# Kernel tuning notes

Measured on AMD Instinct MI355X. Metric: run time of the kernel, lower is better.

Reference implementation:

```python
import jax, jax.numpy as jnp
import numpy as np

C = 64          # out_C
IN_C = 2 * C    # in_C
B, H, W = 4, 64, 64


def conv_bn_relu(x, w, s, b):
    # 3x3 conv (stride 1, pad 1, no bias) + folded BatchNorm affine + ReLU
    y = jax.lax.conv_general_dilated(
        x, w, window_strides=(1, 1), padding=((1, 1), (1, 1)),
        dimension_numbers=("NCHW", "OIHW", "NCHW"))
    return jax.nn.relu(y * s[None, :, None, None] + b[None, :, None, None])


def attend(K, V, Q):
    # K, V, Q: [B, C, H, W]; mask = softmax(K^T Q) over last dim; out = V @ mask^T
    b, c, h, w = V.shape
    n = h * w
    Kf = K.reshape(b, c, n)
    Vf = V.reshape(b, c, n)
    Qf = Q.reshape(b, c, n)
    mask = jax.nn.softmax(jnp.einsum("bcn,bcm->bnm", Kf, Qf), axis=-1)  # [B,N,N]
    ref = jnp.einsum("bcn,bmn->bcm", Vf, mask)                          # V @ mask^T
    return ref.reshape(b, c, h, w)


def _conv_params(key, cin, cout):
    k1, k2, k3 = jax.random.split(key, 3)
    w = jax.random.normal(k1, (cout, cin, 3, 3), jnp.float32) * (1.0 / np.sqrt(cin * 9))
    s = jax.random.uniform(k2, (cout,), jnp.float32, 0.5, 1.5)   # folded BN scale
    bb = jax.random.normal(k3, (cout,), jnp.float32) * 0.1       # folded BN shift
    return w, s, bb


def setup_inputs() -> dict:
    key = jax.random.key(0)
    ks = jax.random.split(key, 9)
    x = jax.random.normal(ks[0], (B, C, H, W), jnp.float32)
    y = jax.random.normal(ks[1], (B, C, H, W), jnp.float32)
    q_w, q_s, q_b = _conv_params(ks[2], IN_C, C)
    rk_w, rk_s, rk_b = _conv_params(ks[3], C, C)
    rv_w, rv_s, rv_b = _conv_params(ks[4], C, C)
    ik_w, ik_s, ik_b = _conv_params(ks[5], C, C)
    iv_w, iv_s, iv_b = _conv_params(ks[6], C, C)
    sr_w, sr_s, sr_b = _conv_params(ks[7], IN_C, C)
    g1 = jax.random.normal(jax.random.fold_in(ks[8], 1), (1,), jnp.float32) * 0.1
    g2 = jax.random.normal(jax.random.fold_in(ks[8], 2), (1,), jnp.float32) * 0.1
    return dict(x=x, y=y,
                q_w=q_w, q_s=q_s, q_b=q_b,
                rk_w=rk_w, rk_s=rk_s, rk_b=rk_b,
                rv_w=rv_w, rv_s=rv_s, rv_b=rv_b,
                ik_w=ik_w, ik_s=ik_s, ik_b=ik_b,
                iv_w=iv_w, iv_s=iv_s, iv_b=iv_b,
                sr_w=sr_w, sr_s=sr_s, sr_b=sr_b,
                gamma1=g1, gamma2=g2)


def reference(x, y, q_w, q_s, q_b, rk_w, rk_s, rk_b, rv_w, rv_s, rv_b,
              ik_w, ik_s, ik_b, iv_w, iv_s, iv_b, sr_w, sr_s, sr_b,
              gamma1, gamma2):
    Q = conv_bn_relu(jnp.concatenate([x, y], axis=1), q_w, q_s, q_b)
    rgb_k = conv_bn_relu(x, rk_w, rk_s, rk_b)
    rgb_v = conv_bn_relu(x, rv_w, rv_s, rv_b)
    rgb_refine = gamma1[0] * attend(rgb_k, rgb_v, Q) + y
    inf_k = conv_bn_relu(y, ik_w, ik_s, ik_b)
    inf_v = conv_bn_relu(y, iv_w, iv_s, iv_b)
    inf_refine = gamma2[0] * attend(inf_k, inf_v, Q) + x
    out = conv_bn_relu(jnp.concatenate([rgb_refine, inf_refine], axis=1), sr_w, sr_s, sr_b)
    return out
```

## Files before the change

kernel.cpp:

```cpp
#include <hip/hip_runtime.h>
#include <hip/hip_bf16.h>

#define NPOS 4096
#define CD   64
#define NB   4
#define PADW 66
#define PADN (66*66)
#define NSEG 4
#define NT   (NPOS / NSEG / 64)
#define LOG2E 1.4426950408889634f

extern "C" __device__ float __ocml_exp2_f32(float);

typedef __bf16 bf16x8_t __attribute__((ext_vector_type(8)));
typedef float  f32x4_t  __attribute__((ext_vector_type(4)));

static __device__ __forceinline__ unsigned short f2bf(float f) {
    return __builtin_bit_cast(unsigned short, __float2bfloat16(f));
}

static __device__ __forceinline__ void gload_lds16(const void* g, void* l) {
    __builtin_amdgcn_global_load_lds(
        (const __attribute__((address_space(1))) void*)g,
        (__attribute__((address_space(3))) void*)l, 16, 0, 0);
}

static __device__ __forceinline__ unsigned cvtpk_bf16(float lo, float hi) {
    unsigned r;
    asm("v_cvt_pk_bf16_f32 %0, %1, %2" : "=v"(r) : "v"(lo), "v"(hi));
    return r;
}

__global__ __launch_bounds__(256) void prep_kernel(
    const float* __restrict__ x, const float* __restrict__ y,
    const float* __restrict__ qw, const float* __restrict__ rkw,
    const float* __restrict__ rvw, const float* __restrict__ ikw,
    const float* __restrict__ ivw, const float* __restrict__ srw,
    const float* __restrict__ qs, const float* __restrict__ rks,
    const float* __restrict__ rvs, const float* __restrict__ iks,
    const float* __restrict__ ivs, const float* __restrict__ srs,
    unsigned short* __restrict__ pads, unsigned short* __restrict__ Wf)
{
    const int bx = blockIdx.x;
    if (bx < 16) {
        unsigned short* p = pads + (size_t)bx * PADN * CD;
        const uint4 z = make_uint4(0, 0, 0, 0);
        for (int idx = threadIdx.x; idx < 260 * 8; idx += 256) {
            const int pi = idx >> 3, chn = idx & 7;
            int pos;
            if (pi < 66)       pos = pi;
            else if (pi < 132) pos = 65 * PADW + (pi - 66);
            else { const int rem = pi - 132;
                   pos = (1 + (rem >> 1)) * PADW + ((rem & 1) ? 65 : 0); }
            *(uint4*)(p + (size_t)pos * CD + chn * 8) = z;
        }
        return;
    }
    if (bx < 160) {
        const int f = bx - 16;
        const float* w; const float* s; int cin, local;
        if (f < 36)       { w = qw;  s = qs;  cin = 128; local = f; }
        else if (f < 54)  { w = rkw; s = rks; cin = 64;  local = f - 36; }
        else if (f < 72)  { w = rvw; s = rvs; cin = 64;  local = f - 54; }
        else if (f < 90)  { w = ikw; s = iks; cin = 64;  local = f - 72; }
        else if (f < 108) { w = ivw; s = ivs; cin = 64;  local = f - 90; }
        else              { w = srw; s = srs; cin = 128; local = f - 108; }
        const int src = (cin == 128) ? local / 18 : 0;
        const int rem = (cin == 128) ? local % 18 : local;
        const int tap = rem >> 1, kt = rem & 1;
        const int t = threadIdx.x, cot = t >> 6, l = t & 63;
        const int co = cot * 16 + (l & 15);
        const float kmul = ((f >= 36 && f < 54) || (f >= 72 && f < 90)) ? LOG2E : 1.0f;
        const float sc = s[co] * kmul;
        unsigned short us[8];
#pragma unroll
        for (int e = 0; e < 8; ++e) {
            const int ci = src * 64 + kt * 32 + ((l >> 4) * 8) + e;
            us[e] = f2bf(w[((size_t)co * cin + ci) * 9 + tap] * sc);
        }
        *(uint4*)(Wf + ((size_t)(f * 4 + cot) * 64 + l) * 8) = *(uint4*)us;
        return;
    }
    {
        const int idx = bx - 160;
        const int h = idx & 63, b = (idx >> 6) & 3, src = idx >> 8;
        const float* in = src ? y : x;
        unsigned short* out = pads + (size_t)src * NB * PADN * CD;
        __shared__ float t[64][65];
        const int tt = threadIdx.x;
        {
            const int ci = tt >> 2, w0 = (tt & 3) * 16;
            const float* p = in + ((size_t)b * 64 + ci) * NPOS + h * 64 + w0;
#pragma unroll
            for (int j = 0; j < 16; j += 4) {
                float4 v = *(const float4*)(p + j);
                t[ci][w0 + j] = v.x; t[ci][w0 + j + 1] = v.y;
                t[ci][w0 + j + 2] = v.z; t[ci][w0 + j + 3] = v.w;
            }
        }
        __syncthreads();
        const int w = tt >> 2, c0 = (tt & 3) * 16;
        unsigned short us[16];
#pragma unroll
        for (int j = 0; j < 16; ++j) us[j] = f2bf(t[c0 + j][w]);
        unsigned short* q = out + ((size_t)b * PADN + (h + 1) * PADW + (w + 1)) * CD + c0;
        *(uint4*)q = *(uint4*)us;
        *(uint4*)(q + 8) = *(uint4*)(us + 8);
    }
}

__global__ __launch_bounds__(256) void conv_mfma_kernel(
    const unsigned short* __restrict__ xpad, const unsigned short* __restrict__ ypad,
    const unsigned short* __restrict__ rpadR, const unsigned short* __restrict__ rpadI,
    const unsigned short* __restrict__ Wf,
    const float* __restrict__ qb, const float* __restrict__ rkb,
    const float* __restrict__ rvb, const float* __restrict__ ikb,
    const float* __restrict__ ivb, const float* __restrict__ srb,
    unsigned short* __restrict__ Qt, unsigned short* __restrict__ KtR,
    unsigned short* __restrict__ VR, unsigned short* __restrict__ KtI,
    unsigned short* __restrict__ VI, float* __restrict__ outf,
    int convid_base)
{
    const int conv = convid_base + (blockIdx.z >> 1);
    const int ch   = blockIdx.z & 1;
    const int rp = blockIdx.x, b = blockIdx.y;
    const unsigned short *in0, *in1; const float* bias;
    int nsrc, wfbase, layout; void* outp;
    switch (conv) {
        case 0:  in0 = xpad;  in1 = ypad;  nsrc = 2; wfbase = 0;   bias = qb;  outp = Qt;  layout = 0; break;
        case 1:  in0 = xpad;  in1 = 0;     nsrc = 1; wfbase = 36;  bias = rkb; outp = KtR; layout = 0; break;
        case 2:  in0 = xpad;  in1 = 0;     nsrc = 1; wfbase = 54;  bias = rvb; outp = VR;  layout = 1; break;
        case 3:  in0 = ypad;  in1 = 0;     nsrc = 1; wfbase = 72;  bias = ikb; outp = KtI; layout = 0; break;
        case 4:  in0 = ypad;  in1 = 0;     nsrc = 1; wfbase = 90;  bias = ivb; outp = VI;  layout = 1; break;
        default: in0 = rpadR; in1 = rpadI; nsrc = 2; wfbase = 108; bias = srb; outp = outf; layout = 2; break;
    }
    const float bmul = (conv == 1 || conv == 3) ? LOG2E : 1.0f;
    const int lane = threadIdx.x & 63, wv = threadIdx.x >> 6;
    const int l15 = lane & 15, g = lane >> 4;
    const int hrow = rp * 2 + (wv >> 1);
    const int posg = (wv & 1) * 32;

    __shared__ unsigned short Wl[12 * 512];

    f32x4_t acc[2][2];
#pragma unroll
    for (int i = 0; i < 2; ++i)
#pragma unroll
        for (int j = 0; j < 2; ++j) acc[i][j] = (f32x4_t){0.f, 0.f, 0.f, 0.f};

    const int nchunk = nsrc * 3;
    for (int c = 0; c < nchunk; ++c) {
        const int src = (c >= 3) ? 1 : 0;
        const int ky  = c - src * 3;
        if (c) __syncthreads();
#pragma unroll
        for (int j = 0; j < 3; ++j) {
            const int slot = wv * 3 + j;
            const int fj = slot >> 1, cotl = slot & 1;
            const int fg = wfbase + c * 6 + fj;
            gload_lds16(Wf + ((size_t)(fg * 4 + ch * 2 + cotl) * 64 + lane) * 8,
                        Wl + slot * 512);
        }
        __syncthreads();
        const unsigned short* base = (src ? in1 : in0) + (size_t)b * PADN * CD;
#pragma unroll
        for (int pf = 0; pf < 2; ++pf) {
#pragma unroll
            for (int kx = 0; kx < 3; ++kx) {
                const int pos = (hrow + ky) * PADW + posg + pf * 16 + kx + l15;
                const unsigned short* ap = base + (size_t)pos * CD + g * 8;
#pragma unroll
                for (int kt = 0; kt < 2; ++kt) {
                    bf16x8_t a = *(const bf16x8_t*)(ap + kt * 32);
                    const int fj = kx * 2 + kt;
#pragma unroll
                    for (int cc = 0; cc < 2; ++cc) {
                        bf16x8_t bfr = *(const bf16x8_t*)(Wl + (size_t)(fj * 2 + cc) * 512 + lane * 8);
                        acc[pf][cc] = __builtin_amdgcn_mfma_f32_16x16x32_bf16(a, bfr, acc[pf][cc], 0, 0, 0);
                    }
                }
            }
        }
    }

#pragma unroll
    for (int pf = 0; pf < 2; ++pf) {
        const int nb4 = hrow * 64 + posg + pf * 16 + g * 4;
        if (layout == 0) {
            unsigned short* o = (unsigned short*)outp + (size_t)b * NPOS * CD;
#pragma unroll
            for (int cc = 0; cc < 2; ++cc) {
                const int co = (ch * 2 + cc) * 16 + l15;
                const float bv = bias[co] * bmul;
#pragma unroll
                for (int r = 0; r < 4; ++r)
                    o[(size_t)(nb4 + r) * CD + co] = f2bf(fmaxf(acc[pf][cc][r] + bv, 0.f));
            }
        } else if (layout == 1) {
            unsigned short* o = (unsigned short*)outp + (size_t)b * CD * NPOS;
#pragma unroll
            for (int cc = 0; cc < 2; ++cc) {
                const int cch = (ch * 2 + cc) * 16 + l15;
                const float bv = bias[cch];
                unsigned short us[4];
#pragma unroll
                for (int r = 0; r < 4; ++r) us[r] = f2bf(fmaxf(acc[pf][cc][r] + bv, 0.f));
                *(uint2*)(o + (size_t)cch * NPOS + nb4) = *(uint2*)us;
            }
        } else {
            float* o = (float*)outp + (size_t)b * CD * NPOS;
#pragma unroll
            for (int cc = 0; cc < 2; ++cc) {
                const int cch = (ch * 2 + cc) * 16 + l15;
                const float bv = bias[cch];
                f32x4_t v;
#pragma unroll
                for (int r = 0; r < 4; ++r) v[r] = fmaxf(acc[pf][cc][r] + bv, 0.f);
                *(f32x4_t*)(o + (size_t)cch * NPOS + nb4) = v;
            }
        }
    }
}

__global__ __launch_bounds__(256) void attn_kernel(
    const unsigned short* __restrict__ Qt,
    const unsigned short* __restrict__ KtR, const unsigned short* __restrict__ KtI,
    const unsigned short* __restrict__ VR,  const unsigned short* __restrict__ VI,
    float* __restrict__ Opart, float* __restrict__ ml)
{
    const int fid = blockIdx.x;
    const int att = fid & 1;
    const int b   = (fid >> 1) & 3;
    const int seg = (fid >> 3) & 3;
    const int mblk = fid >> 5;
    const int lane = threadIdx.x & 63, wv = threadIdx.x >> 6;
    const int l15 = lane & 15, g = lane >> 4;
    const int m0 = mblk * 64 + wv * 16;

    const unsigned short* Qb = Qt + (size_t)b * NPOS * CD;
    const unsigned short* Kb = (att ? KtI : KtR) + (size_t)b * NPOS * CD;
    const unsigned short* Vb = (att ? VI : VR) + (size_t)b * CD * NPOS;

    __shared__ unsigned short Qs[2][64 * 64];
    __shared__ unsigned short Vs[2][64 * 64];
    __shared__ unsigned short plds[4][16 * 68];
    unsigned short* pl = plds[wv];

    const bf16x8_t bK0 = *(const bf16x8_t*)&Kb[(size_t)(m0 + l15) * CD + g * 8];
    const bf16x8_t bK1 = *(const bf16x8_t*)&Kb[(size_t)(m0 + l15) * CD + 32 + g * 8];

    f32x4_t O[4];
#pragma unroll
    for (int i = 0; i < 4; ++i) O[i] = (f32x4_t){0.f, 0.f, 0.f, 0.f};
    float mrun = -3.0e38f, lsum = 0.f;

    const int csw = (lane & 7) ^ ((lane >> 3) & 7);
    const int sx = l15 & 7;
    const int nbase = seg * (NPOS / NSEG);

    const int rq = wv * 16 + (lane >> 3);
    const unsigned short* qsrc0 = Qb + (size_t)(nbase + rq) * CD + csw * 8;
    const unsigned short* qsrc1 = qsrc0 + (size_t)8 * CD;
    const unsigned short* vsrc0 = Vb + (size_t)rq * NPOS + nbase + csw * 8;
    const unsigned short* vsrc1 = vsrc0 + (size_t)8 * NPOS;
    unsigned short* qdst = &Qs[0][(wv * 16) * 64];
    unsigned short* vdst = &Vs[0][(wv * 16) * 64];

#define STAGE(buf, itv) do {                                                  \
        const size_t qo = (size_t)(itv) * (64 * CD);                          \
        const size_t vo = (size_t)(itv) * 64;                                 \
        gload_lds16(qsrc0 + qo, qdst + (buf) * 4096);                         \
        gload_lds16(qsrc1 + qo, qdst + (buf) * 4096 + 512);                   \
        gload_lds16(vsrc0 + vo, vdst + (buf) * 4096);                         \
        gload_lds16(vsrc1 + vo, vdst + (buf) * 4096 + 512);                   \
    } while (0)

    STAGE(0, 0);

    for (int it = 0; it < NT; ++it) {
        const int cur = it & 1;
        __syncthreads();
        if (it + 1 < NT) STAGE(cur ^ 1, it + 1);

        f32x4_t St[4];
        __builtin_amdgcn_s_setprio(1);
#pragma unroll
        for (int nt = 0; nt < 4; ++nt) {
            const unsigned short* qr = &Qs[cur][(nt * 16 + l15) * 64];
            bf16x8_t a0 = *(const bf16x8_t*)(qr + (g ^ sx) * 8);
            bf16x8_t a1 = *(const bf16x8_t*)(qr + ((4 + g) ^ sx) * 8);
            f32x4_t c = (f32x4_t){0.f, 0.f, 0.f, 0.f};
            c = __builtin_amdgcn_mfma_f32_16x16x32_bf16(a0, bK0, c, 0, 0, 0);
            c = __builtin_amdgcn_mfma_f32_16x16x32_bf16(a1, bK1, c, 0, 0, 0);
            St[nt] = c;
        }
        __builtin_amdgcn_s_setprio(0);

        float tmax = St[0][0];
#pragma unroll
        for (int nt = 0; nt < 4; ++nt) {
            tmax = fmaxf(fmaxf(tmax, St[nt][0]), St[nt][1]);
            tmax = fmaxf(fmaxf(tmax, St[nt][2]), St[nt][3]);
        }
        if (!__all(tmax <= mrun + 12.0f)) {
            float tr = fmaxf(tmax, __shfl_xor(tmax, 16));
            tr = fmaxf(tr, __shfl_xor(tr, 32));
            const float mnew = fmaxf(mrun, tr);
            const float corr = __builtin_amdgcn_exp2f(mrun - mnew);
            lsum *= corr;
#pragma unroll
            for (int i = 0; i < 4; ++i) {
                O[i][0] *= corr; O[i][1] *= corr; O[i][2] *= corr; O[i][3] *= corr;
            }
            mrun = mnew;
        }
        unsigned int pw[8];
#pragma unroll
        for (int nt = 0; nt < 4; ++nt) {
            float p0 = __builtin_amdgcn_exp2f(St[nt][0] - mrun);
            float p1 = __builtin_amdgcn_exp2f(St[nt][1] - mrun);
            float p2 = __builtin_amdgcn_exp2f(St[nt][2] - mrun);
            float p3 = __builtin_amdgcn_exp2f(St[nt][3] - mrun);
            lsum += (p0 + p1) + (p2 + p3);
            pw[nt * 2 + 0] = cvtpk_bf16(p0, p1);
            pw[nt * 2 + 1] = cvtpk_bf16(p2, p3);
        }
#pragma unroll
        for (int nt = 0; nt < 4; ++nt)
            *(uint2*)&pl[l15 * 68 + nt * 16 + g * 4] =
                make_uint2(pw[nt * 2], pw[nt * 2 + 1]);

        __builtin_amdgcn_s_setprio(1);
#pragma unroll
        for (int nc = 0; nc < 2; ++nc) {
            union { bf16x8_t v; uint2 d2[2]; } bp;
            bp.d2[0] = *(uint2*)&pl[l15 * 68 + nc * 32 + g * 8];
            bp.d2[1] = *(uint2*)&pl[l15 * 68 + nc * 32 + g * 8 + 4];
#pragma unroll
            for (int ct = 0; ct < 4; ++ct) {
                bf16x8_t av = *(const bf16x8_t*)
                    (&Vs[cur][(ct * 16 + l15) * 64 + (((nc * 4 + g) ^ sx) * 8)]);
                O[ct] = __builtin_amdgcn_mfma_f32_16x16x32_bf16(av, bp.v, O[ct], 0, 0, 0);
            }
        }
        __builtin_amdgcn_s_setprio(0);
    }

    float lred = lsum + __shfl_xor(lsum, 16);
    lred += __shfl_xor(lred, 32);
    float* Ob = Opart + ((((size_t)att * NB + b) * NSEG + seg) * NPOS) * CD;
    const int m = m0 + l15;
#pragma unroll
    for (int ct = 0; ct < 4; ++ct)
        *(f32x4_t*)(Ob + (size_t)m * CD + ct * 16 + g * 4) = O[ct];
    if (g == 0) {
        float* mlb = ml + ((((size_t)att * NB + b) * NSEG + seg) * NPOS + m) * 2;
        mlb[0] = mrun; mlb[1] = lred;
    }
#undef STAGE
}

__global__ __launch_bounds__(256) void combine_kernel(
    const float* __restrict__ Opart, const float* __restrict__ ml,
    const float* __restrict__ x, const float* __restrict__ y,
    const float* __restrict__ g1, const float* __restrict__ g2,
    unsigned short* __restrict__ rpadR, unsigned short* __restrict__ rpadI)
{
    const int mt = blockIdx.x, b = blockIdx.y, att = blockIdx.z;
    const float* resid = att ? x : y;
    const float gamma = att ? g2[0] : g1[0];
    unsigned short* rp = (att ? rpadI : rpadR) + (size_t)b * PADN * CD;
    __shared__ float t[64][17];
    const int tt = threadIdx.x;
    {
        const int c = tt >> 2, m4 = (tt & 3) * 4;
        const float4 v = *(const float4*)(resid + ((size_t)b * CD + c) * NPOS + mt * 16 + m4);
        t[c][m4] = v.x; t[c][m4 + 1] = v.y; t[c][m4 + 2] = v.z; t[c][m4 + 3] = v.w;
    }
    __syncthreads();
    const int c = tt & 63, mq = tt >> 6;
    const size_t ob = (((size_t)att * NB + b) * NSEG) * NPOS * CD;
    const size_t mb = (((size_t)att * NB + b) * NSEG) * NPOS;
#pragma unroll
    for (int p = 0; p < 4; ++p) {
        const int mloc = mq * 4 + p;
        const int m = mt * 16 + mloc;
        float mm[NSEG], llv[NSEG];
#pragma unroll
        for (int s = 0; s < NSEG; ++s) {
            mm[s] = ml[(mb + (size_t)s * NPOS + m) * 2];
            llv[s] = ml[(mb + (size_t)s * NPOS + m) * 2 + 1];
        }
        float M = mm[0];
#pragma unroll
        for (int s = 1; s < NSEG; ++s) M = fmaxf(M, mm[s]);
        float Ov = 0.f, L = 0.f;
#pragma unroll
        for (int s = 0; s < NSEG; ++s) {
            const float wgt = __ocml_exp2_f32(mm[s] - M);
            L += wgt * llv[s];
            Ov += wgt * Opart[ob + ((size_t)s * NPOS + m) * CD + c];
        }
        const float val = fmaf(gamma, Ov / L, t[c][mloc]);
        const int h = m >> 6, w_ = m & 63;
        rp[((size_t)((h + 1) * PADW) + (w_ + 1)) * CD + c] = f2bf(val);
    }
}

extern "C" void kernel_launch(void* const* d_in, const int* in_sizes, int n_in,
                              void* d_out, int out_size, void* d_ws, size_t ws_size,
                              hipStream_t stream)
{
    const float* x    = (const float*)d_in[0];
    const float* y    = (const float*)d_in[1];
    const float* q_w  = (const float*)d_in[2];
    const float* q_s  = (const float*)d_in[3];
    const float* q_b  = (const float*)d_in[4];
    const float* rk_w = (const float*)d_in[5];
    const float* rk_s = (const float*)d_in[6];
    const float* rk_b = (const float*)d_in[7];
    const float* rv_w = (const float*)d_in[8];
    const float* rv_s = (const float*)d_in[9];
    const float* rv_b = (const float*)d_in[10];
    const float* ik_w = (const float*)d_in[11];
    const float* ik_s = (const float*)d_in[12];
    const float* ik_b = (const float*)d_in[13];
    const float* iv_w = (const float*)d_in[14];
    const float* iv_s = (const float*)d_in[15];
    const float* iv_b = (const float*)d_in[16];
    const float* sr_w = (const float*)d_in[17];
    const float* sr_s = (const float*)d_in[18];
    const float* sr_b = (const float*)d_in[19];
    const float* g1   = (const float*)d_in[20];
    const float* g2   = (const float*)d_in[21];

    char* ws = (char*)d_ws;
    size_t off = 0;
    auto alloc = [&](size_t bytes) {
        void* p = ws + off; off += (bytes + 255) & ~(size_t)255; return p;
    };
    const size_t PADB = (size_t)NB * PADN * CD * 2;
    unsigned short* xpad  = (unsigned short*)alloc(PADB);
    unsigned short* ypad  = (unsigned short*)alloc(PADB);
    unsigned short* rpadR = (unsigned short*)alloc(PADB);
    unsigned short* rpadI = (unsigned short*)alloc(PADB);
    unsigned short* Qt  = (unsigned short*)alloc((size_t)NB * NPOS * CD * 2);
    unsigned short* KtR = (unsigned short*)alloc((size_t)NB * NPOS * CD * 2);
    unsigned short* KtI = (unsigned short*)alloc((size_t)NB * NPOS * CD * 2);
    unsigned short* VR  = (unsigned short*)alloc((size_t)NB * NPOS * CD * 2);
    unsigned short* VI  = (unsigned short*)alloc((size_t)NB * NPOS * CD * 2);
    unsigned short* Wf  = (unsigned short*)alloc((size_t)144 * 4 * 64 * 16);
    float* Opart = (float*)alloc((size_t)2 * NB * NSEG * NPOS * CD * 4);
    float* mlb   = (float*)alloc((size_t)2 * NB * NSEG * NPOS * 2 * 4);

    prep_kernel<<<dim3(672), 256, 0, stream>>>(
        x, y, q_w, rk_w, rv_w, ik_w, iv_w, sr_w,
        q_s, rk_s, rv_s, ik_s, iv_s, sr_s, xpad, Wf);
    conv_mfma_kernel<<<dim3(32, NB, 10), 256, 0, stream>>>(
        xpad, ypad, rpadR, rpadI, Wf,
        q_b, rk_b, rv_b, ik_b, iv_b, sr_b,
        Qt, KtR, VR, KtI, VI, nullptr, 0);
    attn_kernel<<<dim3(64 * NB * 2 * NSEG), 256, 0, stream>>>(
        Qt, KtR, KtI, VR, VI, Opart, mlb);
    combine_kernel<<<dim3(256, NB, 2), 256, 0, stream>>>(
        Opart, mlb, x, y, g1, g2, rpadR, rpadI);
    conv_mfma_kernel<<<dim3(32, NB, 2), 256, 0, stream>>>(
        xpad, ypad, rpadR, rpadI, Wf,
        q_b, rk_b, rv_b, ik_b, iv_b, sr_b,
        Qt, KtR, VR, KtI, VI, (float*)d_out, 5);
}
```

Baseline: 220.2 us.

## Stage all 3x3 conv weights per source once and drop Q LDS staging in attention

The conv kernel now loads all nine taps of weights for a source into LDS in one go, and each block computes four output rows. This cuts the number of barriers and weight reloads per block and halves the grid. The attention kernel stops staging Q tiles through LDS and reads Q fragments straight from global memory, which removes LDS traffic and synchronisation work but depends on cache hits for the direct global reads. The larger weight buffer raises LDS use in the conv kernel and fewer blocks may lower occupancy.

```diff
diff --git a/kernel.cpp b/kernel.cpp
--- a/kernel.cpp
+++ b/kernel.cpp
@@ -123,7 +123,7 @@
 {
     const int conv = convid_base + (blockIdx.z >> 1);
     const int ch   = blockIdx.z & 1;
-    const int rp = blockIdx.x, b = blockIdx.y;
+    const int hg = blockIdx.x, b = blockIdx.y;
     const unsigned short *in0, *in1; const float* bias;
     int nsrc, wfbase, layout; void* outp;
     switch (conv) {
@@ -137,46 +137,44 @@
     const float bmul = (conv == 1 || conv == 3) ? LOG2E : 1.0f;
     const int lane = threadIdx.x & 63, wv = threadIdx.x >> 6;
     const int l15 = lane & 15, g = lane >> 4;
-    const int hrow = rp * 2 + (wv >> 1);
-    const int posg = (wv & 1) * 32;
-
-    __shared__ unsigned short Wl[12 * 512];
-
-    f32x4_t acc[2][2];
-#pragma unroll
-    for (int i = 0; i < 2; ++i)
+
+    __shared__ unsigned short Wl[36 * 512];
+
+    f32x4_t acc[4][2];
+#pragma unroll
+    for (int i = 0; i < 4; ++i)
 #pragma unroll
         for (int j = 0; j < 2; ++j) acc[i][j] = (f32x4_t){0.f, 0.f, 0.f, 0.f};
 
-    const int nchunk = nsrc * 3;
-    for (int c = 0; c < nchunk; ++c) {
-        const int src = (c >= 3) ? 1 : 0;
-        const int ky  = c - src * 3;
-        if (c) __syncthreads();
-#pragma unroll
-        for (int j = 0; j < 3; ++j) {
-            const int slot = wv * 3 + j;
-            const int fj = slot >> 1, cotl = slot & 1;
-            const int fg = wfbase + c * 6 + fj;
-            gload_lds16(Wf + ((size_t)(fg * 4 + ch * 2 + cotl) * 64 + lane) * 8,
+    for (int src = 0; src < nsrc; ++src) {
+        if (src) __syncthreads();
+#pragma unroll
+        for (int j = 0; j < 9; ++j) {
+            const int slot = wv * 9 + j;
+            const int fg = wfbase + src * 18 + (slot >> 1);
+            gload_lds16(Wf + ((size_t)(fg * 4 + ch * 2 + (slot & 1)) * 64 + lane) * 8,
                         Wl + slot * 512);
         }
         __syncthreads();
         const unsigned short* base = (src ? in1 : in0) + (size_t)b * PADN * CD;
 #pragma unroll
-        for (int pf = 0; pf < 2; ++pf) {
-#pragma unroll
-            for (int kx = 0; kx < 3; ++kx) {
-                const int pos = (hrow + ky) * PADW + posg + pf * 16 + kx + l15;
-                const unsigned short* ap = base + (size_t)pos * CD + g * 8;
-#pragma unroll
-                for (int kt = 0; kt < 2; ++kt) {
-                    bf16x8_t a = *(const bf16x8_t*)(ap + kt * 32);
-                    const int fj = kx * 2 + kt;
-#pragma unroll
-                    for (int cc = 0; cc < 2; ++cc) {
-                        bf16x8_t bfr = *(const bf16x8_t*)(Wl + (size_t)(fj * 2 + cc) * 512 + lane * 8);
-                        acc[pf][cc] = __builtin_amdgcn_mfma_f32_16x16x32_bf16(a, bfr, acc[pf][cc], 0, 0, 0);
+        for (int r = 0; r < 4; ++r) {
+            const int hrow = hg * 4 + r;
+#pragma unroll
+            for (int ky = 0; ky < 3; ++ky) {
+#pragma unroll
+                for (int kx = 0; kx < 3; ++kx) {
+                    const int pos = (hrow + ky) * PADW + wv * 16 + kx + l15;
+                    const unsigned short* ap = base + (size_t)pos * CD + g * 8;
+#pragma unroll
+                    for (int kt = 0; kt < 2; ++kt) {
+                        bf16x8_t a = *(const bf16x8_t*)(ap + kt * 32);
+                        const int fl = (ky * 3 + kx) * 2 + kt;
+#pragma unroll
+                        for (int cc = 0; cc < 2; ++cc) {
+                            bf16x8_t bfr = *(const bf16x8_t*)(Wl + (size_t)(fl * 2 + cc) * 512 + lane * 8);
+                            acc[r][cc] = __builtin_amdgcn_mfma_f32_16x16x32_bf16(a, bfr, acc[r][cc], 0, 0, 0);
+                        }
                     }
                 }
             }
@@ -184,8 +182,8 @@
     }
 
 #pragma unroll
-    for (int pf = 0; pf < 2; ++pf) {
-        const int nb4 = hrow * 64 + posg + pf * 16 + g * 4;
+    for (int r = 0; r < 4; ++r) {
+        const int nb4 = (hg * 4 + r) * 64 + wv * 16 + g * 4;
         if (layout == 0) {
             unsigned short* o = (unsigned short*)outp + (size_t)b * NPOS * CD;
 #pragma unroll
@@ -193,8 +191,8 @@
                 const int co = (ch * 2 + cc) * 16 + l15;
                 const float bv = bias[co] * bmul;
 #pragma unroll
-                for (int r = 0; r < 4; ++r)
-                    o[(size_t)(nb4 + r) * CD + co] = f2bf(fmaxf(acc[pf][cc][r] + bv, 0.f));
+                for (int rr = 0; rr < 4; ++rr)
+                    o[(size_t)(nb4 + rr) * CD + co] = f2bf(fmaxf(acc[r][cc][rr] + bv, 0.f));
             }
         } else if (layout == 1) {
             unsigned short* o = (unsigned short*)outp + (size_t)b * CD * NPOS;
@@ -204,7 +202,7 @@
                 const float bv = bias[cch];
                 unsigned short us[4];
 #pragma unroll
-                for (int r = 0; r < 4; ++r) us[r] = f2bf(fmaxf(acc[pf][cc][r] + bv, 0.f));
+                for (int rr = 0; rr < 4; ++rr) us[rr] = f2bf(fmaxf(acc[r][cc][rr] + bv, 0.f));
                 *(uint2*)(o + (size_t)cch * NPOS + nb4) = *(uint2*)us;
             }
         } else {
@@ -215,7 +213,7 @@
                 const float bv = bias[cch];
                 f32x4_t v;
 #pragma unroll
-                for (int r = 0; r < 4; ++r) v[r] = fmaxf(acc[pf][cc][r] + bv, 0.f);
+                for (int rr = 0; rr < 4; ++rr) v[rr] = fmaxf(acc[r][cc][rr] + bv, 0.f);
                 *(f32x4_t*)(o + (size_t)cch * NPOS + nb4) = v;
             }
         }
@@ -241,7 +239,6 @@
     const unsigned short* Kb = (att ? KtI : KtR) + (size_t)b * NPOS * CD;
     const unsigned short* Vb = (att ? VI : VR) + (size_t)b * CD * NPOS;
 
-    __shared__ unsigned short Qs[2][64 * 64];
     __shared__ unsigned short Vs[2][64 * 64];
     __shared__ unsigned short plds[4][16 * 68];
     unsigned short* pl = plds[wv];
@@ -259,36 +256,32 @@
     const int nbase = seg * (NPOS / NSEG);
 
     const int rq = wv * 16 + (lane >> 3);
-    const unsigned short* qsrc0 = Qb + (size_t)(nbase + rq) * CD + csw * 8;
-    const unsigned short* qsrc1 = qsrc0 + (size_t)8 * CD;
     const unsigned short* vsrc0 = Vb + (size_t)rq * NPOS + nbase + csw * 8;
     const unsigned short* vsrc1 = vsrc0 + (size_t)8 * NPOS;
-    unsigned short* qdst = &Qs[0][(wv * 16) * 64];
     unsigned short* vdst = &Vs[0][(wv * 16) * 64];
 
-#define STAGE(buf, itv) do {                                                  \
-        const size_t qo = (size_t)(itv) * (64 * CD);                          \
+#define STAGE_V(buf, itv) do {                                                \
         const size_t vo = (size_t)(itv) * 64;                                 \
-        gload_lds16(qsrc0 + qo, qdst + (buf) * 4096);                         \
-        gload_lds16(qsrc1 + qo, qdst + (buf) * 4096 + 512);                   \
         gload_lds16(vsrc0 + vo, vdst + (buf) * 4096);                         \
         gload_lds16(vsrc1 + vo, vdst + (buf) * 4096 + 512);                   \
     } while (0)
 
-    STAGE(0, 0);
+    STAGE_V(0, 0);
+
+    const unsigned short* qrow = Qb + (size_t)(nbase + l15) * CD + g * 8;
 
     for (int it = 0; it < NT; ++it) {
         const int cur = it & 1;
         __syncthreads();
-        if (it + 1 < NT) STAGE(cur ^ 1, it + 1);
-
+        if (it + 1 < NT) STAGE_V(cur ^ 1, it + 1);
+
+        const unsigned short* qp = qrow + (size_t)it * 64 * CD;
         f32x4_t St[4];
         __builtin_amdgcn_s_setprio(1);
 #pragma unroll
         for (int nt = 0; nt < 4; ++nt) {
-            const unsigned short* qr = &Qs[cur][(nt * 16 + l15) * 64];
-            bf16x8_t a0 = *(const bf16x8_t*)(qr + (g ^ sx) * 8);
-            bf16x8_t a1 = *(const bf16x8_t*)(qr + ((4 + g) ^ sx) * 8);
+            bf16x8_t a0 = *(const bf16x8_t*)(qp + (size_t)(nt * 16) * CD);
+            bf16x8_t a1 = *(const bf16x8_t*)(qp + (size_t)(nt * 16) * CD + 32);
             f32x4_t c = (f32x4_t){0.f, 0.f, 0.f, 0.f};
             c = __builtin_amdgcn_mfma_f32_16x16x32_bf16(a0, bK0, c, 0, 0, 0);
             c = __builtin_amdgcn_mfma_f32_16x16x32_bf16(a1, bK1, c, 0, 0, 0);
@@ -357,7 +350,7 @@
         float* mlb = ml + ((((size_t)att * NB + b) * NSEG + seg) * NPOS + m) * 2;
         mlb[0] = mrun; mlb[1] = lred;
     }
-#undef STAGE
+#undef STAGE_V
 }
 
 __global__ __launch_bounds__(256) void combine_kernel(
@@ -456,7 +449,7 @@
     prep_kernel<<<dim3(672), 256, 0, stream>>>(
         x, y, q_w, rk_w, rv_w, ik_w, iv_w, sr_w,
         q_s, rk_s, rv_s, ik_s, iv_s, sr_s, xpad, Wf);
-    conv_mfma_kernel<<<dim3(32, NB, 10), 256, 0, stream>>>(
+    conv_mfma_kernel<<<dim3(16, NB, 10), 256, 0, stream>>>(
         xpad, ypad, rpadR, rpadI, Wf,
         q_b, rk_b, rv_b, ik_b, iv_b, sr_b,
         Qt, KtR, VR, KtI, VI, nullptr, 0);
@@ -464,7 +457,7 @@
         Qt, KtR, KtI, VR, VI, Opart, mlb);
     combine_kernel<<<dim3(256, NB, 2), 256, 0, stream>>>(
         Opart, mlb, x, y, g1, g2, rpadR, rpadI);
-    conv_mfma_kernel<<<dim3(32, NB, 2), 256, 0, stream>>>(
+    conv_mfma_kernel<<<dim3(16, NB, 2), 256, 0, stream>>>(
         xpad, ypad, rpadR, rpadI, Wf,
         q_b, rk_b, rv_b, ik_b, iv_b, sr_b,
         Qt, KtR, VR, KtI, VI, (float*)d_out, 5);
```

Result: slower. 272.7 us (+23.8%).
